# Performance work log

Measured on AMD Instinct MI355X. Metric: run time of the kernel, lower is better.

Reference implementation:

```python
import jax, jax.numpy as jnp
import numpy as np

K = 5            # srn kernel size (kernels[0])
EPSILON = 1e-3   # epsilons -> SRN additive noise scale
BN_EPS = 1e-5
NUM_SLICES = 3
OUT_CH = 64
CLASSES = 5


def _unfold(x, k):
    # torch.nn.Unfold, padding=0: (B, C*k*k, L), channel-major then (kh, kw) row-major
    B, C, H, W = x.shape
    Ho, Wo = H - k + 1, W - k + 1
    cols = jnp.stack([x[:, :, i:i + Ho, j:j + Wo]
                      for i in range(k) for j in range(k)], axis=2)  # (B,C,k*k,Ho,Wo)
    return cols.reshape(B, C * k * k, Ho * Wo), Ho, Wo


def _bn(x, g, b):
    # BatchNorm2d in training mode: batch statistics, biased variance
    m = x.mean((0, 2, 3), keepdims=True)
    v = x.var((0, 2, 3), keepdims=True)
    return (x - m) * jax.lax.rsqrt(v + BN_EPS) * g[None, :, None, None] + b[None, :, None, None]


def _conv(x, w, b):
    y = jax.lax.conv_general_dilated(x, w, (1, 1), 'VALID',
                                     dimension_numbers=('NCHW', 'OIHW', 'NCHW'))
    return y + b[None, :, None, None]


def _avgpool(x, s):
    B, C, H, W = x.shape
    return x.reshape(B, C, H // s, s, W // s, s).mean((3, 5))


def _maxpool(x, s):
    B, C, H, W = x.shape
    return x.reshape(B, C, H // s, s, W // s, s).max((3, 5))


def _srn(x, srn_w):
    B = x.shape[0]
    y, Ho, Wo = _unfold(x, K)                               # (B, n, L)
    y = y + EPSILON * jax.random.normal(jax.random.key(42), y.shape, y.dtype)
    gg = jnp.std(y, axis=1, ddof=1, keepdims=True)          # torch.std is unbiased
    y = y / gg
    O, C, _, _, S = srn_w.shape
    n = C * K * K
    X = srn_w.reshape(O, n, S)
    X = jnp.concatenate([jnp.ones((O, n, 1), X.dtype), X], axis=2)   # (O, n, S+1)
    Xcov = jnp.einsum('onf,ong->ofg', X, X)                 # X^T X, (O, 4, 4)
    Xinv = jnp.linalg.inv(Xcov)
    M = jnp.einsum('ofg,ong->ofn', Xinv, X)
    Wc = jnp.einsum('ofn,bnl->bofl', M, y)
    pred = jnp.einsum('onf,bofl->bonl', X, Wc)              # fitted values (B,O,n,L)
    err = jnp.mean((y[:, None] - pred) ** 2, axis=2)        # (B,O,L)
    err = err.reshape(B, O, Ho, Wo)
    A = (jnp.exp(-err) - np.exp(-1.0)) / (1.0 - np.exp(-1.0))
    return A - 0.5


def setup_inputs() -> dict:
    key = jax.random.key(0)
    ks = jax.random.split(key, 12)
    x = jax.random.normal(ks[0], (4, 3, 64, 64), jnp.float32)
    # xavier-style init scaled up for numerical stability of the small-matrix inverse
    srn_w = 0.05 * jax.random.normal(ks[1], (OUT_CH, 3, K, K, NUM_SLICES), jnp.float32)
    conv2_w = 0.05 * jax.random.normal(ks[2], (128, 64, 3, 3), jnp.float32)
    conv2_b = 0.01 * jax.random.normal(ks[3], (128,), jnp.float32)
    conv3_w = 0.05 * jax.random.normal(ks[4], (128, 128, 3, 3), jnp.float32)
    conv3_b = 0.01 * jax.random.normal(ks[5], (128,), jnp.float32)
    conv4_w = 0.05 * jax.random.normal(ks[6], (128, 128, 3, 3), jnp.float32)
    conv4_b = 0.01 * jax.random.normal(ks[7], (128,), jnp.float32)
    bn1_g = jnp.ones((64,), jnp.float32); bn1_b = jnp.zeros((64,), jnp.float32)
    bn2_g = jnp.ones((128,), jnp.float32); bn2_b = jnp.zeros((128,), jnp.float32)
    bn3_g = jnp.ones((128,), jnp.float32); bn3_b = jnp.zeros((128,), jnp.float32)
    bn4_g = jnp.ones((128,), jnp.float32); bn4_b = jnp.zeros((128,), jnp.float32)
    fc2_w = 0.05 * jax.random.normal(ks[8], (CLASSES, 128, 1, 1), jnp.float32)
    fc2_b = 0.01 * jax.random.normal(ks[9], (CLASSES,), jnp.float32)
    return dict(x=x, srn_w=srn_w, conv2_w=conv2_w, conv2_b=conv2_b,
                conv3_w=conv3_w, conv3_b=conv3_b, conv4_w=conv4_w, conv4_b=conv4_b,
                bn1_g=bn1_g, bn1_b=bn1_b, bn2_g=bn2_g, bn2_b=bn2_b,
                bn3_g=bn3_g, bn3_b=bn3_b, bn4_g=bn4_g, bn4_b=bn4_b,
                fc2_w=fc2_w, fc2_b=fc2_b)


def reference(x, srn_w, conv2_w, conv2_b, conv3_w, conv3_b, conv4_w, conv4_b,
              bn1_g, bn1_b, bn2_g, bn2_b, bn3_g, bn3_b, bn4_g, bn4_b,
              fc2_w, fc2_b):
    h = _srn(x, srn_w)                                      # (B,64,60,60)
    h = _avgpool(h, 2)
    h = _bn(h, bn1_g, bn1_b)
    h = jax.nn.relu(_bn(_conv(h, conv2_w, conv2_b), bn2_g, bn2_b))
    h = _avgpool(h, 2)
    h = jax.nn.relu(_bn(_conv(h, conv3_w, conv3_b), bn3_g, bn3_b))
    h = _maxpool(h, 2)
    h = jax.nn.relu(_bn(_conv(h, conv4_w, conv4_b), bn4_g, bn4_b))
    h = _maxpool(h, 4)                                      # (B,128,1,1)
    flat = h.reshape(h.shape[0], -1)                        # (B,128)
    return flat @ fc2_w.reshape(CLASSES, -1).T + fc2_b      # 1x1 conv == matmul
```

## Files before the change

kernel.cpp:

```cpp
#include <hip/hip_runtime.h>
#include <math.h>

__device__ __align__(16) float g_w2p[16 * 1152 * 4];
__device__ __align__(16) float g_w3p[32 * 1152 * 4];
__device__ __align__(16) float g_w4p[8 * 4608 * 4];
__device__ __align__(16) float g_h1[4 * 30 * 30 * 64];
__device__ __align__(16) float g_h2[4 * 14 * 14 * 4 * 128];
__device__ __align__(16) float g_h3[4 * 6 * 6 * 4 * 128];
__device__ __align__(16) float g_h4[4 * 16 * 128];

__global__ __launch_bounds__(256) void k_srn(const float* __restrict__ x,
                                             const float* __restrict__ srn_w,
                                             const float* __restrict__ w2,
                                             float* __restrict__ stats) {
    __shared__ __align__(16) float wlds[64 * 244];
    __shared__ float xsm[648];
    __shared__ float part[2 * 15 * 66];
    __shared__ float redS[256], redQ[256];
    int bid = blockIdx.x, t = threadIdx.x;
    int b = bid / 60, rem = bid % 60, r = rem >> 1, ch = rem & 1;

    for (int j = bid * 256 + t; j < 73728; j += 240 * 256) {
        int c = j & 3, s4 = j >> 2;
        int sl = s4 % 36, tmp = s4 / 36, oc_l = tmp & 31, blk = tmp >> 5;
        int it = blk & 3, ocg = blk >> 2;
        int kw = sl % 3, icq = (sl / 3) & 3, kh = sl / 12;
        int ic = it * 16 + icq * 4 + c;
        g_w2p[j] = w2[((ocg * 32 + oc_l) * 64 + ic) * 9 + kh * 3 + kw];
    }

    float4 wr[15];
#pragma unroll
    for (int k = 0; k < 15; k++) {
        int i4 = k * 256 + t;
        if (i4 < 3600) wr[k] = ((const float4*)srn_w)[i4];
    }
    float xr[3];
#pragma unroll
    for (int k = 0; k < 3; k++) {
        int i = t + k * 256;
        if (i < 648) {
            int c = i / 216, rm = i % 216, rr = rm / 36, col = rm % 36;
            int gc = ch * 30 + col; if (gc > 63) gc = 63;
            xr[k] = x[((b * 3 + c) * 64 + (2 * r + rr)) * 64 + gc];
        }
    }
#pragma unroll
    for (int k = 0; k < 15; k++) {
        int i4 = k * 256 + t;
        if (i4 < 3600) {
            float v4[4] = { wr[k].x, wr[k].y, wr[k].z, wr[k].w };
#pragma unroll
            for (int e = 0; e < 4; e++) {
                int i = i4 * 4 + e, o = i / 225, jj = i % 225;
                wlds[o * 244 + (jj / 15) * 16 + (jj % 15)] = v4[e];
            }
        }
    }
#pragma unroll
    for (int k = 0; k < 3; k++) { int i = t + k * 256; if (i < 648) xsm[i] = xr[k]; }
    __syncthreads();

    int w = t >> 6, o = t & 63;
    int rw = w & 1, cq = w >> 1, base = cq * 16;

    float z1[16], z2[16], z3[16], s[16], q[16];
#pragma unroll
    for (int i = 0; i < 16; i++) { z1[i]=0; z2[i]=0; z3[i]=0; s[i]=0; q[i]=0; }

    for (int c = 0; c < 3; c++) {
#pragma unroll
        for (int kh = 0; kh < 5; kh++) {
            float xv[20];
#pragma unroll
            for (int k = 0; k < 20; k++) xv[k] = xsm[(c * 6 + rw + kh) * 36 + base + k];
            float wf[16];
            const float* wp = &wlds[o * 244 + (c * 5 + kh) * 16];
            *(float4*)&wf[0]  = *(const float4*)&wp[0];
            *(float4*)&wf[4]  = *(const float4*)&wp[4];
            *(float4*)&wf[8]  = *(const float4*)&wp[8];
            *(float4*)&wf[12] = *(const float4*)&wp[12];
#pragma unroll
            for (int kw = 0; kw < 5; kw++) {
                float w1 = wf[kw * 3], w2v = wf[kw * 3 + 1], w3v = wf[kw * 3 + 2];
#pragma unroll
                for (int i = 0; i < 16; i++) {
                    float v = xv[kw + i];
                    s[i] += v; q[i] += v * v;
                    z1[i] += w1 * v; z2[i] += w2v * v; z3[i] += w3v * v;
                }
            }
        }
    }

    float gm[16];
    {
        float c01=0,c02=0,c03=0,c11=0,c12=0,c13=0,c22=0,c23=0,c33=0;
#pragma unroll
        for (int row = 0; row < 15; row++) {
            float wf[16];
            const float* wp = &wlds[o * 244 + row * 16];
            *(float4*)&wf[0]  = *(const float4*)&wp[0];
            *(float4*)&wf[4]  = *(const float4*)&wp[4];
            *(float4*)&wf[8]  = *(const float4*)&wp[8];
            *(float4*)&wf[12] = *(const float4*)&wp[12];
#pragma unroll
            for (int kw = 0; kw < 5; kw++) {
                float w1 = wf[kw*3], w2v = wf[kw*3+1], w3v = wf[kw*3+2];
                c01 += w1; c02 += w2v; c03 += w3v;
                c11 += w1*w1; c12 += w1*w2v; c13 += w1*w3v;
                c22 += w2v*w2v; c23 += w2v*w3v; c33 += w3v*w3v;
            }
        }
        float A[4][8];
        A[0][0]=75.f; A[0][1]=c01; A[0][2]=c02; A[0][3]=c03;
        A[1][0]=c01;  A[1][1]=c11; A[1][2]=c12; A[1][3]=c13;
        A[2][0]=c02;  A[2][1]=c12; A[2][2]=c22; A[2][3]=c23;
        A[3][0]=c03;  A[3][1]=c13; A[3][2]=c23; A[3][3]=c33;
#pragma unroll
        for (int i = 0; i < 4; i++)
#pragma unroll
            for (int j = 0; j < 4; j++) A[i][4 + j] = (i == j) ? 1.f : 0.f;
#pragma unroll
        for (int p = 0; p < 4; p++) {
            float ip = 1.f / A[p][p];
#pragma unroll
            for (int j = 0; j < 8; j++) A[p][j] *= ip;
#pragma unroll
            for (int i = 0; i < 4; i++) if (i != p) {
                float f = A[i][p];
#pragma unroll
                for (int j = 0; j < 8; j++) A[i][j] -= f * A[p][j];
            }
        }
#pragma unroll
        for (int i = 0; i < 4; i++)
#pragma unroll
            for (int j = 0; j < 4; j++) gm[i * 4 + j] = A[i][4 + j];
    }

    const float C1 = 0.36787944117144233f;
    const float INV = 1.5819767068693265f;
#pragma unroll
    for (int pp = 0; pp < 8; pp++) {
        int pl = cq * 8 + pp;
        if (pl < 15) {
            float aa = 0.f;
#pragma unroll
            for (int e = 0; e < 2; e++) {
                int i = 2 * pp + e;
                float sum = s[i], sq = q[i];
                float gg2 = (sq - sum * sum * (1.f / 75.f)) * (1.f / 74.f);
                float zf[4] = { sum, z1[i], z2[i], z3[i] };
                float qf = 0.f;
#pragma unroll
                for (int f = 0; f < 4; f++) {
                    float acc = 0.f;
#pragma unroll
                    for (int h = 0; h < 4; h++) acc += gm[f * 4 + h] * zf[h];
                    qf += acc * zf[f];
                }
                float err = (sq - qf) / (75.f * gg2);
                aa += (expf(-err) - C1) * INV - 0.5f;
            }
            part[(rw * 15 + pl) * 66 + o] = 0.25f * aa;
        }
    }
    __syncthreads();

    int j2 = t >> 6;
    float ps = 0.f, pq = 0.f;
    for (int pl = j2; pl < 15; pl += 4) {
        float v = part[pl * 66 + o] + part[(15 + pl) * 66 + o];
        g_h1[((b * 30 + r) * 30 + ch * 15 + pl) * 64 + o] = v;
        ps += v; pq += v * v;
    }
    redS[t] = ps; redQ[t] = pq;
    __syncthreads();
    if (t < 64) {
        atomicAdd(&stats[t],      redS[t] + redS[64 + t] + redS[128 + t] + redS[192 + t]);
        atomicAdd(&stats[64 + t], redQ[t] + redQ[64 + t] + redQ[128 + t] + redQ[192 + t]);
    }
}

__global__ __launch_bounds__(256) void k_conv2(const float* __restrict__ w3,
                                               const float* __restrict__ w4,
                                               const float* __restrict__ g1,
                                               const float* __restrict__ b1,
                                               float* __restrict__ stats) {
    __shared__ __align__(16) float ws[2 * 32 * 148];
    __shared__ __align__(16) float xs[3 * 16 * 64];
    __shared__ float redS[256], redQ[256];
    int blk = blockIdx.x, t = threadIdx.x;
    int b = blk / 224, rem = blk % 224, oh = rem >> 3, sub = rem & 7;
    int owh = sub >> 2, ocg = sub & 3;
    int oc_l = t & 31, grp = t >> 5;
    int now = (grp < 6) ? 2 : 1;
    int lowb = (grp < 6) ? grp * 2 : 12 + (grp - 6);

    {
        int j = blk * 256 + t;
        if (j < 147456) {
            int c = j & 3, s4 = j >> 2;
            int sl = s4 % 36, tmp = s4 / 36, oc2 = tmp & 31, bk = tmp >> 5;
            int it = bk & 7, og = bk >> 3;
            int kw = sl % 3, icq = (sl / 3) & 3, kh = sl / 12;
            int ic = it * 16 + icq * 4 + c;
            g_w3p[j] = w3[((og * 32 + oc2) * 128 + ic) * 9 + kh * 3 + kw];
        }
    }
    {
        int j = blk * 256 + t;
        if (j < 147456) {
            int c = j & 3, s4 = j >> 2;
            int sl = s4 % 72, tmp = s4 / 72, oc2 = tmp & 15, blkq = tmp >> 4;
            int icq = blkq & 3, og = blkq >> 2;
            int kw = sl % 3, icb2 = (sl / 3) & 7, kh = sl / 24;
            int ic = icq * 32 + icb2 * 4 + c;
            g_w4p[j] = w4[((og * 16 + oc2) * 128 + ic) * 9 + kh * 3 + kw];
        }
    }

    const float4* wsrc = (const float4*)g_w2p + (ocg * 4) * 1152;
    {
        int icb = (t & 15) * 4;
        float4 S = *(const float4*)&stats[icb], Q = *(const float4*)&stats[64 + icb];
        float4 G4 = *(const float4*)&g1[icb], B4 = *(const float4*)&b1[icb];
        float scv[4], shv[4];
        float mm[4] = { S.x, S.y, S.z, S.w }, qq[4] = { Q.x, Q.y, Q.z, Q.w };
        float gg[4] = { G4.x, G4.y, G4.z, G4.w }, bb[4] = { B4.x, B4.y, B4.z, B4.w };
#pragma unroll
        for (int c = 0; c < 4; c++) {
            float m = mm[c] * (1.f / 3600.f);
            float v = qq[c] * (1.f / 3600.f) - m * m;
            scv[c] = gg[c] * rsqrtf(v + 1e-5f);
            shv[c] = bb[c] - m * scv[c];
        }
        int px = t >> 4, ic4 = t & 15;
        float4 xr[3];
#pragma unroll
        for (int k = 0; k < 3; k++)
            xr[k] = ((const float4*)g_h1)[((b * 30 + oh + k) * 30 + owh * 14 + px) * 16 + ic4];
        float4 wreg[9];
#pragma unroll
        for (int k = 0; k < 9; k++) wreg[k] = wsrc[k * 256 + t];
#pragma unroll
        for (int k = 0; k < 3; k++) {
            float4 v;
            v.x = xr[k].x * scv[0] + shv[0]; v.y = xr[k].y * scv[1] + shv[1];
            v.z = xr[k].z * scv[2] + shv[2]; v.w = xr[k].w * scv[3] + shv[3];
            *(float4*)&xs[((k * 16 + px) * 16 + ic4) * 4] = v;
        }
#pragma unroll
        for (int k = 0; k < 9; k++) {
            int idx = k * 256 + t;
            int tile = idx / 1152, r2 = idx % 1152;
            *(float4*)&ws[tile * 4736 + (r2 / 36) * 148 + (r2 % 36) * 4] = wreg[k];
        }
    }
    __syncthreads();

    float acc[2] = {0, 0};
    for (int rr = 0; rr < 2; ++rr) {
        float4 wreg[9];
        if (rr == 0) {
#pragma unroll
            for (int k = 0; k < 9; k++) wreg[k] = wsrc[2 * 1152 + k * 256 + t];
        }
        for (int half = 0; half < 2; ++half) {
            int it = rr * 2 + half;
            const float* wB = &ws[half * 4736 + oc_l * 148];
#pragma unroll 1
            for (int icq = 0; icq < 4; icq++) {
                int xoff = it * 16 + icq * 4;
#pragma unroll
                for (int kh = 0; kh < 3; kh++) {
                    const float* wb = &wB[(kh * 4 + icq) * 12];
                    float4 w0 = *(const float4*)&wb[0];
                    float4 w1 = *(const float4*)&wb[4];
                    float4 w2v = *(const float4*)&wb[8];
                    const float* xrow = &xs[(kh * 16 + lowb) * 64 + xoff];
                    float4 x0 = *(const float4*)&xrow[0];
                    float4 x1 = *(const float4*)&xrow[64];
#pragma unroll
                    for (int i = 0; i < 2; i++) {
                        if (i < now) {
                            float4 x2 = *(const float4*)&xrow[(i + 2) * 64];
                            acc[i] += w0.x * x0.x + w0.y * x0.y + w0.z * x0.z + w0.w * x0.w
                                    + w1.x * x1.x + w1.y * x1.y + w1.z * x1.z + w1.w * x1.w
                                    + w2v.x * x2.x + w2v.y * x2.y + w2v.z * x2.z + w2v.w * x2.w;
                            x0 = x1; x1 = x2;
                        }
                    }
                }
            }
        }
        if (rr == 0) {
            __syncthreads();
#pragma unroll
            for (int k = 0; k < 9; k++) {
                int idx = k * 256 + t;
                int tile = idx / 1152, r2 = idx % 1152;
                *(float4*)&ws[tile * 4736 + (r2 / 36) * 148 + (r2 % 36) * 4] = wreg[k];
            }
            __syncthreads();
        }
    }
    int oc = ocg * 32 + oc_l;
    float ps = 0.f, pq = 0.f;
#pragma unroll
    for (int i = 0; i < 2; i++) {
        if (i < now) {
            int ow = owh * 14 + lowb + i;
            g_h2[(((b * 14 + (oh >> 1)) * 14 + (ow >> 1)) * 4 + (oh & 1) * 2 + (ow & 1)) * 128 + oc] = acc[i];
            ps += acc[i]; pq += acc[i] * acc[i];
        }
    }
    redS[t] = ps; redQ[t] = pq;
    __syncthreads();
    if (t < 32) {
        float aS = 0.f, aQ = 0.f;
#pragma unroll
        for (int k = 0; k < 8; k++) { aS += redS[t + 32 * k]; aQ += redQ[t + 32 * k]; }
        atomicAdd(&stats[128 + ocg * 32 + t], aS);
        atomicAdd(&stats[256 + ocg * 32 + t], aQ);
    }
}

__global__ __launch_bounds__(256) void k_conv3(const float* __restrict__ g2,
                                               const float* __restrict__ b2,
                                               float* __restrict__ stats) {
    __shared__ __align__(16) float ws[2 * 32 * 148];
    __shared__ __align__(16) float xs[3 * 14 * 128];
    __shared__ float redS[256], redQ[256];
    int blk = blockIdx.x, t = threadIdx.x;
    int b = blk / 48, rem = blk % 48, oh = rem >> 2, ocg = rem & 3;
    int oc_l = t & 31, grp = t >> 5;
    int now = (grp < 4) ? 2 : 1;
    int lowb = (grp < 4) ? grp * 2 : 8 + (grp - 4);

    const float4* wsrc = (const float4*)g_w3p + (ocg * 8) * 1152;
    {
        int icb = (t & 31) * 4;
        float4 S = *(const float4*)&stats[128 + icb], Q = *(const float4*)&stats[256 + icb];
        float4 G4 = *(const float4*)&g2[icb], B4 = *(const float4*)&b2[icb];
        float scv[4], shv[4];
        float mm[4] = { S.x, S.y, S.z, S.w }, qq[4] = { Q.x, Q.y, Q.z, Q.w };
        float gg[4] = { G4.x, G4.y, G4.z, G4.w }, bb[4] = { B4.x, B4.y, B4.z, B4.w };
#pragma unroll
        for (int c = 0; c < 4; c++) {
            float m = mm[c] * (1.f / 3136.f);
            float v = qq[c] * (1.f / 3136.f) - m * m;
            scv[c] = gg[c] * rsqrtf(v + 1e-5f);
            shv[c] = bb[c] - m * scv[c];
        }
        float4 wreg[9];
#pragma unroll
        for (int k = 0; k < 9; k++) wreg[k] = wsrc[k * 256 + t];
        float4 pa[6], pb[6], pc[6], pd[6];
#pragma unroll
        for (int k = 0; k < 6; k++) {
            int i4 = t + k * 256;
            if (i4 < 1344) {
                int px = (i4 >> 5) % 14, rr2 = i4 / 448;
                const float4* p0 = (const float4*)&g_h2[(((b * 14 + oh + rr2) * 14 + px) * 4) * 128 + (i4 & 31) * 4];
                pa[k] = p0[0]; pb[k] = p0[32]; pc[k] = p0[64]; pd[k] = p0[96];
            }
        }
#pragma unroll
        for (int k = 0; k < 9; k++) {
            int idx = k * 256 + t;
            int tile = idx / 1152, r2 = idx % 1152;
            *(float4*)&ws[tile * 4736 + (r2 / 36) * 148 + (r2 % 36) * 4] = wreg[k];
        }
#pragma unroll
        for (int k = 0; k < 6; k++) {
            int i4 = t + k * 256;
            if (i4 < 1344) {
                float4 o4;
                o4.x = 0.25f * (fmaxf(pa[k].x * scv[0] + shv[0], 0.f) + fmaxf(pb[k].x * scv[0] + shv[0], 0.f)
                              + fmaxf(pc[k].x * scv[0] + shv[0], 0.f) + fmaxf(pd[k].x * scv[0] + shv[0], 0.f));
                o4.y = 0.25f * (fmaxf(pa[k].y * scv[1] + shv[1], 0.f) + fmaxf(pb[k].y * scv[1] + shv[1], 0.f)
                              + fmaxf(pc[k].y * scv[1] + shv[1], 0.f) + fmaxf(pd[k].y * scv[1] + shv[1], 0.f));
                o4.z = 0.25f * (fmaxf(pa[k].z * scv[2] + shv[2], 0.f) + fmaxf(pb[k].z * scv[2] + shv[2], 0.f)
                              + fmaxf(pc[k].z * scv[2] + shv[2], 0.f) + fmaxf(pd[k].z * scv[2] + shv[2], 0.f));
                o4.w = 0.25f * (fmaxf(pa[k].w * scv[3] + shv[3], 0.f) + fmaxf(pb[k].w * scv[3] + shv[3], 0.f)
                              + fmaxf(pc[k].w * scv[3] + shv[3], 0.f) + fmaxf(pd[k].w * scv[3] + shv[3], 0.f));
                *(float4*)&xs[i4 * 4] = o4;
            }
        }
    }
    __syncthreads();

    float acc[2] = {0, 0};
    for (int rr = 0; rr < 4; ++rr) {
        float4 wreg[9];
        if (rr < 3) {
#pragma unroll
            for (int k = 0; k < 9; k++) wreg[k] = wsrc[(2 * rr + 2) * 1152 + k * 256 + t];
        }
        for (int half = 0; half < 2; ++half) {
            int it = rr * 2 + half;
            const float* wB = &ws[half * 4736 + oc_l * 148];
#pragma unroll 1
            for (int icq = 0; icq < 4; icq++) {
                int xoff = it * 16 + icq * 4;
#pragma unroll
                for (int kh = 0; kh < 3; kh++) {
                    const float* wb = &wB[(kh * 4 + icq) * 12];
                    float4 w0 = *(const float4*)&wb[0];
                    float4 w1 = *(const float4*)&wb[4];
                    float4 w2v = *(const float4*)&wb[8];
                    const float* xrow = &xs[(kh * 14 + lowb) * 128 + xoff];
                    float4 x0 = *(const float4*)&xrow[0];
                    float4 x1 = *(const float4*)&xrow[128];
#pragma unroll
                    for (int i = 0; i < 2; i++) {
                        if (i < now) {
                            float4 x2 = *(const float4*)&xrow[(i + 2) * 128];
                            acc[i] += w0.x * x0.x + w0.y * x0.y + w0.z * x0.z + w0.w * x0.w
                                    + w1.x * x1.x + w1.y * x1.y + w1.z * x1.z + w1.w * x1.w
                                    + w2v.x * x2.x + w2v.y * x2.y + w2v.z * x2.z + w2v.w * x2.w;
                            x0 = x1; x1 = x2;
                        }
                    }
                }
            }
        }
        if (rr < 3) {
            __syncthreads();
#pragma unroll
            for (int k = 0; k < 9; k++) {
                int idx = k * 256 + t;
                int tile = idx / 1152, r2 = idx % 1152;
                *(float4*)&ws[tile * 4736 + (r2 / 36) * 148 + (r2 % 36) * 4] = wreg[k];
            }
            __syncthreads();
        }
    }
    int oc = ocg * 32 + oc_l;
    float ps = 0.f, pq = 0.f;
#pragma unroll
    for (int i = 0; i < 2; i++) {
        if (i < now) {
            int ow = lowb + i;
            g_h3[(((b * 6 + (oh >> 1)) * 6 + (ow >> 1)) * 4 + (oh & 1) * 2 + (ow & 1)) * 128 + oc] = acc[i];
            ps += acc[i]; pq += acc[i] * acc[i];
        }
    }
    redS[t] = ps; redQ[t] = pq;
    __syncthreads();
    if (t < 32) {
        float aS = 0.f, aQ = 0.f;
#pragma unroll
        for (int k = 0; k < 8; k++) { aS += redS[t + 32 * k]; aQ += redQ[t + 32 * k]; }
        atomicAdd(&stats[384 + ocg * 32 + t], aS);
        atomicAdd(&stats[512 + ocg * 32 + t], aQ);
    }
}

__global__ __launch_bounds__(256) void k_conv4(const float* __restrict__ g3,
                                               const float* __restrict__ b3,
                                               float* __restrict__ stats) {
    __shared__ __align__(16) float ws[64 * 292];
    __shared__ __align__(16) float xs[3 * 6 * 128];
    __shared__ float red[256];
    int blk = blockIdx.x, t = threadIdx.x;
    int b = blk / 32, rem = blk % 32, oh = rem / 8, ocg = rem % 8;
    int oc_l = t & 15, ow = (t >> 4) & 3, icq = t >> 6;

    {
        int icb = (t & 31) * 4;
        float4 S = *(const float4*)&stats[384 + icb], Q = *(const float4*)&stats[512 + icb];
        float4 G4 = *(const float4*)&g3[icb], B4 = *(const float4*)&b3[icb];
        float scv[4], shv[4];
        float mm[4] = { S.x, S.y, S.z, S.w }, qq[4] = { Q.x, Q.y, Q.z, Q.w };
        float gg[4] = { G4.x, G4.y, G4.z, G4.w }, bb[4] = { B4.x, B4.y, B4.z, B4.w };
#pragma unroll
        for (int c = 0; c < 4; c++) {
            float m = mm[c] * (1.f / 576.f);
            float v = qq[c] * (1.f / 576.f) - m * m;
            scv[c] = gg[c] * rsqrtf(v + 1e-5f);
            shv[c] = bb[c] - m * scv[c];
        }
        const float4* wsrc = (const float4*)g_w4p + ocg * 4608;
        float4 wreg[18];
#pragma unroll
        for (int k = 0; k < 18; k++) wreg[k] = wsrc[k * 256 + t];
        float4 pa[3], pb[3], pc[3], pd[3];
#pragma unroll
        for (int k = 0; k < 3; k++) {
            int i4 = t + k * 256;
            if (i4 < 576) {
                int px = (i4 >> 5) % 6, rr = i4 / 192;
                const float4* p0 = (const float4*)&g_h3[(((b * 6 + oh + rr) * 6 + px) * 4) * 128 + (i4 & 31) * 4];
                pa[k] = p0[0]; pb[k] = p0[32]; pc[k] = p0[64]; pd[k] = p0[96];
            }
        }
#pragma unroll
        for (int k = 0; k < 18; k++) {
            int idx = k * 256 + t;
            *(float4*)&ws[(idx / 72) * 292 + (idx % 72) * 4] = wreg[k];
        }
#pragma unroll
        for (int k = 0; k < 3; k++) {
            int i4 = t + k * 256;
            if (i4 < 576) {
                float4 o4;
                o4.x = fmaxf(fmaxf(fmaxf(pa[k].x * scv[0] + shv[0], pb[k].x * scv[0] + shv[0]),
                                   fmaxf(pc[k].x * scv[0] + shv[0], pd[k].x * scv[0] + shv[0])), 0.f);
                o4.y = fmaxf(fmaxf(fmaxf(pa[k].y * scv[1] + shv[1], pb[k].y * scv[1] + shv[1]),
                                   fmaxf(pc[k].y * scv[1] + shv[1], pd[k].y * scv[1] + shv[1])), 0.f);
                o4.z = fmaxf(fmaxf(fmaxf(pa[k].z * scv[2] + shv[2], pb[k].z * scv[2] + shv[2]),
                                   fmaxf(pc[k].z * scv[2] + shv[2], pd[k].z * scv[2] + shv[2])), 0.f);
                o4.w = fmaxf(fmaxf(fmaxf(pa[k].w * scv[3] + shv[3], pb[k].w * scv[3] + shv[3]),
                                   fmaxf(pc[k].w * scv[3] + shv[3], pd[k].w * scv[3] + shv[3])), 0.f);
                *(float4*)&xs[i4 * 4] = o4;
            }
        }
    }
    __syncthreads();

    float acc = 0.f;
    const float* wbase = &ws[(icq * 16 + oc_l) * 292];
#pragma unroll 1
    for (int icbq = 0; icbq < 8; icbq++) {
#pragma unroll
        for (int kh = 0; kh < 3; kh++) {
            const float* wb = &wbase[(kh * 8 + icbq) * 12];
            float4 w0 = *(const float4*)&wb[0];
            float4 w1 = *(const float4*)&wb[4];
            float4 w2v = *(const float4*)&wb[8];
            float4 x0 = *(const float4*)&xs[(kh * 6 + ow) * 128 + icq * 32 + icbq * 4];
            float4 x1 = *(const float4*)&xs[(kh * 6 + ow + 1) * 128 + icq * 32 + icbq * 4];
            float4 x2 = *(const float4*)&xs[(kh * 6 + ow + 2) * 128 + icq * 32 + icbq * 4];
            acc += w0.x * x0.x + w0.y * x0.y + w0.z * x0.z + w0.w * x0.w
                 + w1.x * x1.x + w1.y * x1.y + w1.z * x1.z + w1.w * x1.w
                 + w2v.x * x2.x + w2v.y * x2.y + w2v.z * x2.z + w2v.w * x2.w;
        }
    }
    red[t] = acc;
    __syncthreads();
    if (t < 64) {
        float v = red[t] + red[t + 64] + red[t + 128] + red[t + 192];
        int oc = ocg * 16 + (t & 15);
        g_h4[((b * 4 + oh) * 4 + (t >> 4)) * 128 + oc] = v;
        float ps = v + __shfl_xor(v, 16);  ps += __shfl_xor(ps, 32);
        float pv = v * v;
        float pq = pv + __shfl_xor(pv, 16); pq += __shfl_xor(pq, 32);
        if (t < 16) {
            atomicAdd(&stats[640 + ocg * 16 + t], ps);
            atomicAdd(&stats[768 + ocg * 16 + t], pq);
        }
    }
}

__global__ __launch_bounds__(256) void k_final(const float* __restrict__ g4,
                                               const float* __restrict__ b4,
                                               const float* __restrict__ fcw,
                                               const float* __restrict__ fcb,
                                               const float* __restrict__ stats,
                                               float* __restrict__ out) {
    __shared__ float sc[128], sh[128];
    __shared__ float pooled[4][128];
    int t = threadIdx.x;
    if (t < 128) {
        float m = stats[640 + t] * (1.f / 64.f);
        float v = stats[768 + t] * (1.f / 64.f) - m * m;
        float rs = rsqrtf(v + 1e-5f);
        sc[t] = g4[t] * rs; sh[t] = b4[t] - m * sc[t];
    }
    __syncthreads();
    for (int item = t; item < 512; item += 256) {
        int bb = item >> 7, oc = item & 127;
        float s = sc[oc], h = sh[oc];
        float mx = 0.f;
#pragma unroll
        for (int k = 0; k < 16; k++) mx = fmaxf(mx, g_h4[(bb * 16 + k) * 128 + oc] * s + h);
        pooled[bb][oc] = mx;
    }
    __syncthreads();
    if (t < 20) {
        int bb = t / 5, cls = t % 5;
        float acc = fcb[cls];
        const float* w = &fcw[cls * 128];
        for (int oc = 0; oc < 128; oc++) acc += pooled[bb][oc] * w[oc];
        out[bb * 5 + cls] = acc;
    }
}

extern "C" void kernel_launch(void* const* d_in, const int* in_sizes, int n_in,
                              void* d_out, int out_size, void* d_ws, size_t ws_size,
                              hipStream_t stream) {
    (void)in_sizes; (void)n_in; (void)out_size; (void)ws_size;
    const float* x     = (const float*)d_in[0];
    const float* srn_w = (const float*)d_in[1];
    const float* w2    = (const float*)d_in[2];
    const float* w3    = (const float*)d_in[4];
    const float* w4    = (const float*)d_in[6];
    const float* g1 = (const float*)d_in[8];  const float* b1 = (const float*)d_in[9];
    const float* g2 = (const float*)d_in[10]; const float* b2 = (const float*)d_in[11];
    const float* g3 = (const float*)d_in[12]; const float* b3 = (const float*)d_in[13];
    const float* g4 = (const float*)d_in[14]; const float* b4 = (const float*)d_in[15];
    const float* fcw = (const float*)d_in[16]; const float* fcb = (const float*)d_in[17];
    float* out = (float*)d_out;
    float* stats = (float*)d_ws;

    hipMemsetAsync(d_ws, 0, 4096, stream);
    k_srn  <<<dim3(240), dim3(256), 0, stream>>>(x, srn_w, w2, stats);
    k_conv2<<<dim3(896), dim3(256), 0, stream>>>(w3, w4, g1, b1, stats);
    k_conv3<<<dim3(192), dim3(256), 0, stream>>>(g2, b2, stats);
    k_conv4<<<dim3(128), dim3(256), 0, stream>>>(g3, b3, stats);
    k_final<<<dim3(1),   dim3(256), 0, stream>>>(g4, b4, fcw, fcb, stats, out);
}
```

Measured before the change: 101.7 us.

## Double SRN block threads, halve per-thread pixels, fuse Gram accumulation, alias LDS

The SRN kernel now launches 512 threads per block instead of 256. Each thread handles 8 output columns instead of 16, which cuts register pressure and doubles the waves available to hide latency. The Gram-matrix sums are folded into the main accumulation loop, removing a second pass over the weights in LDS. Shared memory is reorganised into one aliased buffer so the partial-result area reuses the weight region, which needs an extra barrier. Every thread in a block still recomputes the same per-channel Gram sums redundantly, and the reduction now spans 8 groups.

```diff
diff --git a/kernel.cpp b/kernel.cpp
--- a/kernel.cpp
+++ b/kernel.cpp
@@ -9,36 +9,41 @@
 __device__ __align__(16) float g_h3[4 * 6 * 6 * 4 * 128];
 __device__ __align__(16) float g_h4[4 * 16 * 128];
 
-__global__ __launch_bounds__(256) void k_srn(const float* __restrict__ x,
+__global__ __launch_bounds__(512) void k_srn(const float* __restrict__ x,
                                              const float* __restrict__ srn_w,
                                              const float* __restrict__ w2,
                                              float* __restrict__ stats) {
-    __shared__ __align__(16) float wlds[64 * 244];
-    __shared__ float xsm[648];
-    __shared__ float part[2 * 15 * 66];
-    __shared__ float redS[256], redQ[256];
+    __shared__ __align__(16) float smem[16264];
+    float* xsm  = smem;
+    float* wlds = smem + 648;
+    float* part = smem + 648;
+    float* redS = smem + 2628;
+    float* redQ = smem + 3140;
     int bid = blockIdx.x, t = threadIdx.x;
     int b = bid / 60, rem = bid % 60, r = rem >> 1, ch = rem & 1;
 
-    for (int j = bid * 256 + t; j < 73728; j += 240 * 256) {
-        int c = j & 3, s4 = j >> 2;
-        int sl = s4 % 36, tmp = s4 / 36, oc_l = tmp & 31, blk = tmp >> 5;
-        int it = blk & 3, ocg = blk >> 2;
-        int kw = sl % 3, icq = (sl / 3) & 3, kh = sl / 12;
-        int ic = it * 16 + icq * 4 + c;
-        g_w2p[j] = w2[((ocg * 32 + oc_l) * 64 + ic) * 9 + kh * 3 + kw];
-    }
-
-    float4 wr[15];
-#pragma unroll
-    for (int k = 0; k < 15; k++) {
-        int i4 = k * 256 + t;
+    {
+        int j = bid * 512 + t;
+        if (j < 73728) {
+            int c = j & 3, s4 = j >> 2;
+            int sl = s4 % 36, tmp = s4 / 36, oc_l = tmp & 31, blk = tmp >> 5;
+            int it = blk & 3, ocg = blk >> 2;
+            int kw = sl % 3, icq = (sl / 3) & 3, kh = sl / 12;
+            int ic = it * 16 + icq * 4 + c;
+            g_w2p[j] = w2[((ocg * 32 + oc_l) * 64 + ic) * 9 + kh * 3 + kw];
+        }
+    }
+
+    float4 wr[8];
+#pragma unroll
+    for (int k = 0; k < 8; k++) {
+        int i4 = k * 512 + t;
         if (i4 < 3600) wr[k] = ((const float4*)srn_w)[i4];
     }
-    float xr[3];
-#pragma unroll
-    for (int k = 0; k < 3; k++) {
-        int i = t + k * 256;
+    float xr[2];
+#pragma unroll
+    for (int k = 0; k < 2; k++) {
+        int i = t + k * 512;
         if (i < 648) {
             int c = i / 216, rm = i % 216, rr = rm / 36, col = rm % 36;
             int gc = ch * 30 + col; if (gc > 63) gc = 63;
@@ -46,8 +51,8 @@
         }
     }
 #pragma unroll
-    for (int k = 0; k < 15; k++) {
-        int i4 = k * 256 + t;
+    for (int k = 0; k < 8; k++) {
+        int i4 = k * 512 + t;
         if (i4 < 3600) {
             float v4[4] = { wr[k].x, wr[k].y, wr[k].z, wr[k].w };
 #pragma unroll
@@ -58,22 +63,23 @@
         }
     }
 #pragma unroll
-    for (int k = 0; k < 3; k++) { int i = t + k * 256; if (i < 648) xsm[i] = xr[k]; }
+    for (int k = 0; k < 2; k++) { int i = t + k * 512; if (i < 648) xsm[i] = xr[k]; }
     __syncthreads();
 
     int w = t >> 6, o = t & 63;
-    int rw = w & 1, cq = w >> 1, base = cq * 16;
-
-    float z1[16], z2[16], z3[16], s[16], q[16];
-#pragma unroll
-    for (int i = 0; i < 16; i++) { z1[i]=0; z2[i]=0; z3[i]=0; s[i]=0; q[i]=0; }
+    int rw = w & 1, cq = w >> 1, base = cq * 8;
+
+    float z1[8], z2[8], z3[8], s[8], q[8];
+#pragma unroll
+    for (int i = 0; i < 8; i++) { z1[i]=0; z2[i]=0; z3[i]=0; s[i]=0; q[i]=0; }
+    float c01=0,c02=0,c03=0,c11=0,c12=0,c13=0,c22=0,c23=0,c33=0;
 
     for (int c = 0; c < 3; c++) {
 #pragma unroll
         for (int kh = 0; kh < 5; kh++) {
-            float xv[20];
-#pragma unroll
-            for (int k = 0; k < 20; k++) xv[k] = xsm[(c * 6 + rw + kh) * 36 + base + k];
+            float xv[12];
+#pragma unroll
+            for (int k = 0; k < 12; k++) xv[k] = xsm[(c * 6 + rw + kh) * 36 + base + k];
             float wf[16];
             const float* wp = &wlds[o * 244 + (c * 5 + kh) * 16];
             *(float4*)&wf[0]  = *(const float4*)&wp[0];
@@ -83,8 +89,11 @@
 #pragma unroll
             for (int kw = 0; kw < 5; kw++) {
                 float w1 = wf[kw * 3], w2v = wf[kw * 3 + 1], w3v = wf[kw * 3 + 2];
-#pragma unroll
-                for (int i = 0; i < 16; i++) {
+                c01 += w1; c02 += w2v; c03 += w3v;
+                c11 += w1 * w1; c12 += w1 * w2v; c13 += w1 * w3v;
+                c22 += w2v * w2v; c23 += w2v * w3v; c33 += w3v * w3v;
+#pragma unroll
+                for (int i = 0; i < 8; i++) {
                     float v = xv[kw + i];
                     s[i] += v; q[i] += v * v;
                     z1[i] += w1 * v; z2[i] += w2v * v; z3[i] += w3v * v;
@@ -95,23 +104,6 @@
 
     float gm[16];
     {
-        float c01=0,c02=0,c03=0,c11=0,c12=0,c13=0,c22=0,c23=0,c33=0;
-#pragma unroll
-        for (int row = 0; row < 15; row++) {
-            float wf[16];
-            const float* wp = &wlds[o * 244 + row * 16];
-            *(float4*)&wf[0]  = *(const float4*)&wp[0];
-            *(float4*)&wf[4]  = *(const float4*)&wp[4];
-            *(float4*)&wf[8]  = *(const float4*)&wp[8];
-            *(float4*)&wf[12] = *(const float4*)&wp[12];
-#pragma unroll
-            for (int kw = 0; kw < 5; kw++) {
-                float w1 = wf[kw*3], w2v = wf[kw*3+1], w3v = wf[kw*3+2];
-                c01 += w1; c02 += w2v; c03 += w3v;
-                c11 += w1*w1; c12 += w1*w2v; c13 += w1*w3v;
-                c22 += w2v*w2v; c23 += w2v*w3v; c33 += w3v*w3v;
-            }
-        }
         float A[4][8];
         A[0][0]=75.f; A[0][1]=c01; A[0][2]=c02; A[0][3]=c03;
         A[1][0]=c01;  A[1][1]=c11; A[1][2]=c12; A[1][3]=c13;
@@ -139,11 +131,13 @@
             for (int j = 0; j < 4; j++) gm[i * 4 + j] = A[i][4 + j];
     }
 
+    __syncthreads();
+
     const float C1 = 0.36787944117144233f;
     const float INV = 1.5819767068693265f;
 #pragma unroll
-    for (int pp = 0; pp < 8; pp++) {
-        int pl = cq * 8 + pp;
+    for (int pp = 0; pp < 4; pp++) {
+        int pl = cq * 4 + pp;
         if (pl < 15) {
             float aa = 0.f;
 #pragma unroll
@@ -170,7 +164,7 @@
 
     int j2 = t >> 6;
     float ps = 0.f, pq = 0.f;
-    for (int pl = j2; pl < 15; pl += 4) {
+    for (int pl = j2; pl < 15; pl += 8) {
         float v = part[pl * 66 + o] + part[(15 + pl) * 66 + o];
         g_h1[((b * 30 + r) * 30 + ch * 15 + pl) * 64 + o] = v;
         ps += v; pq += v * v;
@@ -178,8 +172,11 @@
     redS[t] = ps; redQ[t] = pq;
     __syncthreads();
     if (t < 64) {
-        atomicAdd(&stats[t],      redS[t] + redS[64 + t] + redS[128 + t] + redS[192 + t]);
-        atomicAdd(&stats[64 + t], redQ[t] + redQ[64 + t] + redQ[128 + t] + redQ[192 + t]);
+        float aS = 0.f, aQ = 0.f;
+#pragma unroll
+        for (int k = 0; k < 8; k++) { aS += redS[t + 64 * k]; aQ += redQ[t + 64 * k]; }
+        atomicAdd(&stats[t],      aS);
+        atomicAdd(&stats[64 + t], aQ);
     }
 }
 
@@ -607,7 +604,7 @@
     float* stats = (float*)d_ws;
 
     hipMemsetAsync(d_ws, 0, 4096, stream);
-    k_srn  <<<dim3(240), dim3(256), 0, stream>>>(x, srn_w, w2, stats);
+    k_srn  <<<dim3(240), dim3(512), 0, stream>>>(x, srn_w, w2, stats);
     k_conv2<<<dim3(896), dim3(256), 0, stream>>>(w3, w4, g1, b1, stats);
     k_conv3<<<dim3(192), dim3(256), 0, stream>>>(g2, b2, stats);
     k_conv4<<<dim3(128), dim3(256), 0, stream>>>(g3, b3, stats);
```

Measured after the change: 99.19 us. 1.03x faster.
